# Performance work log

Measured on AMD Instinct MI355X. Metric: run time of the kernel, lower is better.

The kernel has to match this reference:

```python
import jax, jax.numpy as jnp
import numpy as np

B, SQ, SKV, D = 32, 1024, 8192, 64

def setup_inputs() -> dict:
    key = jax.random.key(0)
    kq, kk, kv = jax.random.split(key, 3)
    return {
        "q_local": jax.random.normal(kq, (B, SQ, D), dtype=jnp.float32),
        "k_local": jax.random.normal(kk, (B, SKV, D), dtype=jnp.float32),
        "v_local": jax.random.normal(kv, (B, SKV, D), dtype=jnp.float32),
    }

def reference(q_local, k_local, v_local):
    # Ring attention with online softmax over all ranks' K/V blocks is
    # mathematically identical to unscaled softmax(Q K^T) V over the full KV.
    scores = jnp.einsum("bqd,bkd->bqk", q_local, k_local)  # [B, SQ, SKV]
    weights = jax.nn.softmax(scores, axis=-1)              # stable (max-subtract)
    out = jnp.einsum("bqk,bkd->bqd", weights, v_local)
    return out.astype(q_local.dtype)
```

## Files before the change

kernel.cpp:

```cpp
#include <hip/hip_runtime.h>


#define NBATCH 32
#define SQL 1024
#define SKVL 8192
#define DH 64
#define BM 128
#define BN 64
#define KSTR 72
#define VSTR 72

typedef _Float16 half8 __attribute__((ext_vector_type(8)));
typedef __fp16 fp16x2 __attribute__((ext_vector_type(2)));
typedef float floatx16 __attribute__((ext_vector_type(16)));
typedef float floatx4 __attribute__((ext_vector_type(4)));
typedef unsigned int uint4v __attribute__((ext_vector_type(4)));
typedef unsigned int uint2v __attribute__((ext_vector_type(2)));

union F8U { uint4v u; half8 h; };

#if __has_builtin(__builtin_amdgcn_exp2f)
#define EXP2F(x) __builtin_amdgcn_exp2f(x)
#else
#define EXP2F(x) exp2f(x)
#endif

static __device__ __forceinline__ unsigned pk2(float a, float b) {
#if __has_builtin(__builtin_amdgcn_cvt_pkrtz)
  fp16x2 h = __builtin_amdgcn_cvt_pkrtz(a, b);
  return __builtin_bit_cast(unsigned, h);
#else
  union { _Float16 h[2]; unsigned u; } r;
  r.h[0] = (_Float16)a; r.h[1] = (_Float16)b; return r.u;
#endif
}

#if __has_builtin(__builtin_amdgcn_permlane32_swap)
#define HAVE_PL32 1
static __device__ __forceinline__ void pl32(unsigned& a, unsigned& b) {
  uint2v r = __builtin_amdgcn_permlane32_swap(a, b, false, false);
  a = r[0]; b = r[1];
}
#else
#define HAVE_PL32 0
#endif

template<int NSPLIT>
__global__ __launch_bounds__(256, 3)
void ring_attn(const float* __restrict__ q, const float* __restrict__ k,
               const float* __restrict__ v, float* __restrict__ out,
               float* __restrict__ pO, float* __restrict__ pM, float* __restrict__ pL)
{
  constexpr int NT = SKVL / NSPLIT / BN;
  __shared__ _Float16 Kl[2][BN * KSTR];
  __shared__ _Float16 Vt[2][DH * VSTR];

  const int tid  = threadIdx.x;
  const int lane = tid & 63;
  const int wv   = tid >> 6;
  const int l31  = lane & 31;
  const int hb   = lane >> 5;
  const int b8   = hb * 8;

  int split, batch, qb;
  if (NSPLIT == 4) {
    split = blockIdx.x & 3;
    batch = (blockIdx.x >> 2) & 31;
    qb    = blockIdx.x >> 7;
  } else {
    split = 0;
    batch = blockIdx.x & 31;
    qb    = blockIdx.x >> 5;
  }

  const float* kp = k + ((size_t)batch * SKVL + (size_t)split * (SKVL / NSPLIT)) * DH;
  const float* vp = v + ((size_t)batch * SKVL + (size_t)split * (SKVL / NSPLIT)) * DH;

  const float* qp = q + ((size_t)batch * SQL + qb * BM + wv * 32 + l31) * DH;
  half8 qf[4];
#pragma unroll
  for (int kt = 0; kt < 4; ++kt) {
    float4 a = *(const float4*)(qp + kt * 16 + b8);
    float4 c = *(const float4*)(qp + kt * 16 + b8 + 4);
    float xs[8] = {a.x, a.y, a.z, a.w, c.x, c.y, c.z, c.w};
#pragma unroll
    for (int j = 0; j < 8; ++j)
      qf[kt][j] = (_Float16)(xs[j] * 1.44269504088896340736f);
  }

  const int krt = tid >> 4;
  const int kc  = (tid & 15) * 4;
  const int vnr = 2 * (tid & 31);
  const int vcg = 8 * (tid >> 5);

  float4 gk[4], ga0, ga1, gb0, gb1;
#pragma unroll
  for (int it = 0; it < 4; ++it)
    gk[it] = *(const float4*)(kp + (size_t)(krt + it * 16) * DH + kc);
  ga0 = *(const float4*)(vp + (size_t)vnr * DH + vcg);
  ga1 = *(const float4*)(vp + (size_t)vnr * DH + vcg + 4);
  gb0 = *(const float4*)(vp + (size_t)(vnr + 1) * DH + vcg);
  gb1 = *(const float4*)(vp + (size_t)(vnr + 1) * DH + vcg + 4);

  floatx16 accO[2];
#pragma unroll
  for (int i = 0; i < 2; ++i)
#pragma unroll
    for (int r = 0; r < 16; ++r) accO[i][r] = 0.f;
  float m_run = -3.0e38f, l_run = 0.f;

  int buf = 0;
  for (int tile = 0; tile < NT; ++tile) {
    _Float16* Kb = Kl[buf];
    _Float16* Vb = Vt[buf];

#pragma unroll
    for (int it = 0; it < 4; ++it) {
      uint2 w2 = make_uint2(pk2(gk[it].x, gk[it].y), pk2(gk[it].z, gk[it].w));
      *(uint2*)&Kb[(krt + it * 16) * KSTR + kc] = w2;
    }
    {
      float av[8] = {ga0.x, ga0.y, ga0.z, ga0.w, ga1.x, ga1.y, ga1.z, ga1.w};
      float bv[8] = {gb0.x, gb0.y, gb0.z, gb0.w, gb1.x, gb1.y, gb1.z, gb1.w};
#pragma unroll
      for (int i = 0; i < 8; ++i)
        *(unsigned*)&Vb[(vcg + i) * VSTR + vnr] = pk2(av[i], bv[i]);
    }
    __syncthreads();

    if (tile + 1 < NT) {
      const float* kn = kp + (size_t)(tile + 1) * BN * DH;
      const float* vn = vp + (size_t)(tile + 1) * BN * DH;
#pragma unroll
      for (int it = 0; it < 4; ++it)
        gk[it] = *(const float4*)(kn + (size_t)(krt + it * 16) * DH + kc);
      ga0 = *(const float4*)(vn + (size_t)vnr * DH + vcg);
      ga1 = *(const float4*)(vn + (size_t)vnr * DH + vcg + 4);
      gb0 = *(const float4*)(vn + (size_t)(vnr + 1) * DH + vcg);
      gb1 = *(const float4*)(vn + (size_t)(vnr + 1) * DH + vcg + 4);
    }

    floatx16 st[2];
#pragma unroll
    for (int t = 0; t < 2; ++t)
#pragma unroll
      for (int r = 0; r < 16; ++r) st[t][r] = 0.f;
#pragma unroll
    for (int kt = 0; kt < 4; ++kt) {
#pragma unroll
      for (int t = 0; t < 2; ++t) {
        half8 kf = *(const half8*)&Kb[(t * 32 + l31) * KSTR + kt * 16 + b8];
        st[t] = __builtin_amdgcn_mfma_f32_32x32x16_f16(kf, qf[kt], st[t], 0, 0, 0);
      }
    }

    float mx = -3.0e38f;
#pragma unroll
    for (int t = 0; t < 2; ++t)
#pragma unroll
      for (int r = 0; r < 16; ++r) mx = fmaxf(mx, st[t][r]);
    mx = fmaxf(mx, __shfl_xor(mx, 32, 64));
    float m_new = fmaxf(m_run, mx);
    float alpha = EXP2F(m_run - m_new);
    m_run = m_new;
    float sum = 0.f;
#pragma unroll
    for (int t = 0; t < 2; ++t)
#pragma unroll
      for (int r = 0; r < 16; ++r) {
        float p = EXP2F(st[t][r] - m_new);
        st[t][r] = p;
        sum += p;
      }
    sum += __shfl_xor(sum, 32, 64);
    l_run = alpha * l_run + sum;

    if (__any(alpha != 1.0f)) {
#pragma unroll
      for (int r = 0; r < 16; ++r) {
        int row = (r & 3) + 8 * (r >> 2) + 4 * hb;
        float ar = __shfl(alpha, row, 64);
        accO[0][r] *= ar;
        accO[1][r] *= ar;
      }
    }

#pragma unroll
    for (int t = 0; t < 2; ++t) {
      unsigned P01 = pk2(st[t][0],  st[t][1]);
      unsigned P23 = pk2(st[t][2],  st[t][3]);
      unsigned P45 = pk2(st[t][4],  st[t][5]);
      unsigned P67 = pk2(st[t][6],  st[t][7]);
      unsigned P89 = pk2(st[t][8],  st[t][9]);
      unsigned PAB = pk2(st[t][10], st[t][11]);
      unsigned PCD = pk2(st[t][12], st[t][13]);
      unsigned PEF = pk2(st[t][14], st[t][15]);
      F8U fe, fo;
#if HAVE_PL32
      pl32(P01, P45); fe.u[0] = P01; fe.u[2] = P45;
      pl32(P23, P67); fe.u[1] = P23; fe.u[3] = P67;
      pl32(P89, PCD); fo.u[0] = P89; fo.u[2] = PCD;
      pl32(PAB, PEF); fo.u[1] = PAB; fo.u[3] = PEF;
#else
      unsigned x01 = __shfl_xor(P01, 32, 64), x23 = __shfl_xor(P23, 32, 64);
      unsigned x45 = __shfl_xor(P45, 32, 64), x67 = __shfl_xor(P67, 32, 64);
      unsigned x89 = __shfl_xor(P89, 32, 64), xAB = __shfl_xor(PAB, 32, 64);
      unsigned xCD = __shfl_xor(PCD, 32, 64), xEF = __shfl_xor(PEF, 32, 64);
      fe.u = uint4v{hb ? x45 : P01, hb ? x67 : P23, hb ? P45 : x01, hb ? P67 : x23};
      fo.u = uint4v{hb ? xCD : P89, hb ? xEF : PAB, hb ? PCD : x89, hb ? PEF : xAB};
#endif
#pragma unroll
      for (int ds = 0; ds < 2; ++ds) {
        half8 vf0 = *(const half8*)&Vb[(ds * 32 + l31) * VSTR + (2 * t) * 16 + b8];
        accO[ds] = __builtin_amdgcn_mfma_f32_32x32x16_f16(fe.h, vf0, accO[ds], 0, 0, 0);
        half8 vf1 = *(const half8*)&Vb[(ds * 32 + l31) * VSTR + (2 * t + 1) * 16 + b8];
        accO[ds] = __builtin_amdgcn_mfma_f32_32x32x16_f16(fo.h, vf1, accO[ds], 0, 0, 0);
      }
    }
    buf ^= 1;
  }

  const int rowbase = batch * SQL + qb * BM + wv * 32;
  if (NSPLIT == 1) {
    float linv = 1.0f / l_run;
    float* op = out + (size_t)rowbase * DH;
#pragma unroll
    for (int r = 0; r < 16; ++r) {
      int row = (r & 3) + 8 * (r >> 2) + 4 * hb;
      float lr = __shfl(linv, row, 64);
      op[(size_t)row * DH + l31]      = accO[0][r] * lr;
      op[(size_t)row * DH + 32 + l31] = accO[1][r] * lr;
    }
  } else {
    float* po = pO + ((size_t)split * NBATCH * SQL + rowbase) * DH;
#pragma unroll
    for (int r = 0; r < 16; ++r) {
      int row = (r & 3) + 8 * (r >> 2) + 4 * hb;
      po[(size_t)row * DH + l31]      = accO[0][r];
      po[(size_t)row * DH + 32 + l31] = accO[1][r];
    }
    if (hb == 0) {
      pM[(size_t)split * NBATCH * SQL + rowbase + l31] = m_run;
      pL[(size_t)split * NBATCH * SQL + rowbase + l31] = l_run;
    }
  }
}

__global__ __launch_bounds__(256)
void merge4(const float* __restrict__ pO, const float* __restrict__ pM,
            const float* __restrict__ pL, float* __restrict__ out)
{
  const int i4   = blockIdx.x * 256 + threadIdx.x;
  const int rowg = i4 >> 4;
  const size_t PLANE4 = (size_t)NBATCH * SQL * DH / 4;
  const int    RPL    = NBATCH * SQL;
  float m0 = pM[rowg], m1 = pM[RPL + rowg], m2 = pM[2 * RPL + rowg], m3 = pM[3 * RPL + rowg];
  float mx = fmaxf(fmaxf(m0, m1), fmaxf(m2, m3));
  float w0 = EXP2F(m0 - mx), w1 = EXP2F(m1 - mx), w2 = EXP2F(m2 - mx), w3 = EXP2F(m3 - mx);
  float l = w0 * pL[rowg] + w1 * pL[RPL + rowg] + w2 * pL[2 * RPL + rowg] + w3 * pL[3 * RPL + rowg];
  float li = 1.0f / l;
  const floatx4* p0 = (const floatx4*)pO;
  floatx4 o0 = p0[i4], o1 = p0[PLANE4 + i4], o2 = p0[2 * PLANE4 + i4], o3 = p0[3 * PLANE4 + i4];
  floatx4 o;
#pragma unroll
  for (int j = 0; j < 4; ++j)
    o[j] = (w0 * o0[j] + w1 * o1[j] + w2 * o2[j] + w3 * o3[j]) * li;
  ((floatx4*)out)[i4] = o;
}

extern "C" void kernel_launch(void* const* d_in, const int* in_sizes, int n_in,
                              void* d_out, int out_size, void* d_ws, size_t ws_size,
                              hipStream_t stream) {
  (void)in_sizes; (void)n_in; (void)out_size;
  const float* q = (const float*)d_in[0];
  const float* k = (const float*)d_in[1];
  const float* v = (const float*)d_in[2];
  float* out = (float*)d_out;

  const size_t PLANE = (size_t)NBATCH * SQL * DH;
  const size_t RPL   = (size_t)NBATCH * SQL;
  const size_t need  = (4 * PLANE + 8 * RPL) * sizeof(float);

  if (ws_size >= need) {
    float* pO = (float*)d_ws;
    float* pM = pO + 4 * PLANE;
    float* pL = pM + 4 * RPL;
    ring_attn<4><<<dim3(1024), dim3(256), 0, stream>>>(q, k, v, nullptr, pO, pM, pL);
    merge4<<<dim3((NBATCH * SQL * DH) / 1024), dim3(256), 0, stream>>>(pO, pM, pL, out);
  } else {
    ring_attn<1><<<dim3(256), dim3(256), 0, stream>>>(q, k, v, out, nullptr, nullptr, nullptr);
  }
}
```

Before: 251.9 us.

## Split softmax per 32-key subtile and stage prefetches as packed fp16 to raise occupancy

The online-softmax update now runs per 32-key half tile instead of per 64-key tile, so only one 16-float score accumulator is live at a time. Prefetched K/V values are converted to packed fp16 in registers early, and the V prefetch is staggered to the middle of the tile, lowering peak register pressure. Launch bounds rise from 3 to 4 blocks per SIMD-set to allow higher occupancy. In exchange there are twice as many max/rescale steps per tile, and the prefetch latency is hidden over a shorter window.

```diff
diff --git a/kernel.cpp b/kernel.cpp
--- a/kernel.cpp
+++ b/kernel.cpp
@@ -46,7 +46,7 @@
 #endif
 
 template<int NSPLIT>
-__global__ __launch_bounds__(256, 3)
+__global__ __launch_bounds__(256, 4)
 void ring_attn(const float* __restrict__ q, const float* __restrict__ k,
                const float* __restrict__ v, float* __restrict__ out,
                float* __restrict__ pO, float* __restrict__ pM, float* __restrict__ pL)
@@ -76,6 +76,28 @@
   const float* kp = k + ((size_t)batch * SKVL + (size_t)split * (SKVL / NSPLIT)) * DH;
   const float* vp = v + ((size_t)batch * SKVL + (size_t)split * (SKVL / NSPLIT)) * DH;
 
+  const int krt = tid >> 4;
+  const int kc  = (tid & 15) * 4;
+  const int vnr = 2 * (tid & 31);
+  const int vcg = 8 * (tid >> 5);
+
+  uint2 pkK[4]; unsigned pkV[8];
+  {
+#pragma unroll
+    for (int it = 0; it < 4; ++it) {
+      float4 g = *(const float4*)(kp + (size_t)(krt + it * 16) * DH + kc);
+      pkK[it] = make_uint2(pk2(g.x, g.y), pk2(g.z, g.w));
+    }
+    float4 a0 = *(const float4*)(vp + (size_t)vnr * DH + vcg);
+    float4 a1 = *(const float4*)(vp + (size_t)vnr * DH + vcg + 4);
+    float4 b0 = *(const float4*)(vp + (size_t)(vnr + 1) * DH + vcg);
+    float4 b1 = *(const float4*)(vp + (size_t)(vnr + 1) * DH + vcg + 4);
+    float av[8] = {a0.x, a0.y, a0.z, a0.w, a1.x, a1.y, a1.z, a1.w};
+    float bv[8] = {b0.x, b0.y, b0.z, b0.w, b1.x, b1.y, b1.z, b1.w};
+#pragma unroll
+    for (int i = 0; i < 8; ++i) pkV[i] = pk2(av[i], bv[i]);
+  }
+
   const float* qp = q + ((size_t)batch * SQL + qb * BM + wv * 32 + l31) * DH;
   half8 qf[4];
 #pragma unroll
@@ -88,20 +110,6 @@
       qf[kt][j] = (_Float16)(xs[j] * 1.44269504088896340736f);
   }
 
-  const int krt = tid >> 4;
-  const int kc  = (tid & 15) * 4;
-  const int vnr = 2 * (tid & 31);
-  const int vcg = 8 * (tid >> 5);
-
-  float4 gk[4], ga0, ga1, gb0, gb1;
-#pragma unroll
-  for (int it = 0; it < 4; ++it)
-    gk[it] = *(const float4*)(kp + (size_t)(krt + it * 16) * DH + kc);
-  ga0 = *(const float4*)(vp + (size_t)vnr * DH + vcg);
-  ga1 = *(const float4*)(vp + (size_t)vnr * DH + vcg + 4);
-  gb0 = *(const float4*)(vp + (size_t)(vnr + 1) * DH + vcg);
-  gb1 = *(const float4*)(vp + (size_t)(vnr + 1) * DH + vcg + 4);
-
   floatx16 accO[2];
 #pragma unroll
   for (int i = 0; i < 2; ++i)
@@ -109,92 +117,87 @@
     for (int r = 0; r < 16; ++r) accO[i][r] = 0.f;
   float m_run = -3.0e38f, l_run = 0.f;
 
+  float4 gk[4], gv[4];
   int buf = 0;
   for (int tile = 0; tile < NT; ++tile) {
     _Float16* Kb = Kl[buf];
     _Float16* Vb = Vt[buf];
 
 #pragma unroll
-    for (int it = 0; it < 4; ++it) {
-      uint2 w2 = make_uint2(pk2(gk[it].x, gk[it].y), pk2(gk[it].z, gk[it].w));
-      *(uint2*)&Kb[(krt + it * 16) * KSTR + kc] = w2;
-    }
-    {
-      float av[8] = {ga0.x, ga0.y, ga0.z, ga0.w, ga1.x, ga1.y, ga1.z, ga1.w};
-      float bv[8] = {gb0.x, gb0.y, gb0.z, gb0.w, gb1.x, gb1.y, gb1.z, gb1.w};
-#pragma unroll
-      for (int i = 0; i < 8; ++i)
-        *(unsigned*)&Vb[(vcg + i) * VSTR + vnr] = pk2(av[i], bv[i]);
-    }
+    for (int it = 0; it < 4; ++it)
+      *(uint2*)&Kb[(krt + it * 16) * KSTR + kc] = pkK[it];
+#pragma unroll
+    for (int i = 0; i < 8; ++i)
+      *(unsigned*)&Vb[(vcg + i) * VSTR + vnr] = pkV[i];
     __syncthreads();
 
-    if (tile + 1 < NT) {
+    const bool more = (tile + 1 < NT);
+    if (more) {
       const float* kn = kp + (size_t)(tile + 1) * BN * DH;
-      const float* vn = vp + (size_t)(tile + 1) * BN * DH;
 #pragma unroll
       for (int it = 0; it < 4; ++it)
         gk[it] = *(const float4*)(kn + (size_t)(krt + it * 16) * DH + kc);
-      ga0 = *(const float4*)(vn + (size_t)vnr * DH + vcg);
-      ga1 = *(const float4*)(vn + (size_t)vnr * DH + vcg + 4);
-      gb0 = *(const float4*)(vn + (size_t)(vnr + 1) * DH + vcg);
-      gb1 = *(const float4*)(vn + (size_t)(vnr + 1) * DH + vcg + 4);
-    }
-
-    floatx16 st[2];
-#pragma unroll
-    for (int t = 0; t < 2; ++t)
-#pragma unroll
-      for (int r = 0; r < 16; ++r) st[t][r] = 0.f;
-#pragma unroll
-    for (int kt = 0; kt < 4; ++kt) {
-#pragma unroll
-      for (int t = 0; t < 2; ++t) {
+    }
+
+#pragma unroll
+    for (int t = 0; t < 2; ++t) {
+      floatx16 stv;
+#pragma unroll
+      for (int r = 0; r < 16; ++r) stv[r] = 0.f;
+#pragma unroll
+      for (int kt = 0; kt < 4; ++kt) {
         half8 kf = *(const half8*)&Kb[(t * 32 + l31) * KSTR + kt * 16 + b8];
-        st[t] = __builtin_amdgcn_mfma_f32_32x32x16_f16(kf, qf[kt], st[t], 0, 0, 0);
-      }
-    }
-
-    float mx = -3.0e38f;
-#pragma unroll
-    for (int t = 0; t < 2; ++t)
-#pragma unroll
-      for (int r = 0; r < 16; ++r) mx = fmaxf(mx, st[t][r]);
-    mx = fmaxf(mx, __shfl_xor(mx, 32, 64));
-    float m_new = fmaxf(m_run, mx);
-    float alpha = EXP2F(m_run - m_new);
-    m_run = m_new;
-    float sum = 0.f;
-#pragma unroll
-    for (int t = 0; t < 2; ++t)
+        stv = __builtin_amdgcn_mfma_f32_32x32x16_f16(kf, qf[kt], stv, 0, 0, 0);
+      }
+
+      float mx = stv[0];
+#pragma unroll
+      for (int r = 1; r < 16; ++r) mx = fmaxf(mx, stv[r]);
+      mx = fmaxf(mx, __shfl_xor(mx, 32, 64));
+      float m_new = fmaxf(m_run, mx);
+      float alpha = EXP2F(m_run - m_new);
+      m_run = m_new;
+      float sum = 0.f;
 #pragma unroll
       for (int r = 0; r < 16; ++r) {
-        float p = EXP2F(st[t][r] - m_new);
-        st[t][r] = p;
+        float p = EXP2F(stv[r] - m_new);
+        stv[r] = p;
         sum += p;
       }
-    sum += __shfl_xor(sum, 32, 64);
-    l_run = alpha * l_run + sum;
-
-    if (__any(alpha != 1.0f)) {
-#pragma unroll
-      for (int r = 0; r < 16; ++r) {
-        int row = (r & 3) + 8 * (r >> 2) + 4 * hb;
-        float ar = __shfl(alpha, row, 64);
-        accO[0][r] *= ar;
-        accO[1][r] *= ar;
-      }
-    }
-
-#pragma unroll
-    for (int t = 0; t < 2; ++t) {
-      unsigned P01 = pk2(st[t][0],  st[t][1]);
-      unsigned P23 = pk2(st[t][2],  st[t][3]);
-      unsigned P45 = pk2(st[t][4],  st[t][5]);
-      unsigned P67 = pk2(st[t][6],  st[t][7]);
-      unsigned P89 = pk2(st[t][8],  st[t][9]);
-      unsigned PAB = pk2(st[t][10], st[t][11]);
-      unsigned PCD = pk2(st[t][12], st[t][13]);
-      unsigned PEF = pk2(st[t][14], st[t][15]);
+      sum += __shfl_xor(sum, 32, 64);
+      l_run = alpha * l_run + sum;
+      if (__any(alpha != 1.0f)) {
+#pragma unroll
+        for (int r = 0; r < 16; ++r) {
+          int row = (r & 3) + 8 * (r >> 2) + 4 * hb;
+          float ar = __shfl(alpha, row, 64);
+          accO[0][r] *= ar;
+          accO[1][r] *= ar;
+        }
+      }
+
+      if (more) {
+        if (t == 0) {
+#pragma unroll
+          for (int it = 0; it < 4; ++it)
+            pkK[it] = make_uint2(pk2(gk[it].x, gk[it].y), pk2(gk[it].z, gk[it].w));
+          const float* vn = vp + (size_t)(tile + 1) * BN * DH;
+          gv[0] = *(const float4*)(vn + (size_t)vnr * DH + vcg);
+          gv[1] = *(const float4*)(vn + (size_t)vnr * DH + vcg + 4);
+          gv[2] = *(const float4*)(vn + (size_t)(vnr + 1) * DH + vcg);
+          gv[3] = *(const float4*)(vn + (size_t)(vnr + 1) * DH + vcg + 4);
+        } else {
+          float av[8] = {gv[0].x, gv[0].y, gv[0].z, gv[0].w, gv[1].x, gv[1].y, gv[1].z, gv[1].w};
+          float bv[8] = {gv[2].x, gv[2].y, gv[2].z, gv[2].w, gv[3].x, gv[3].y, gv[3].z, gv[3].w};
+#pragma unroll
+          for (int i = 0; i < 8; ++i) pkV[i] = pk2(av[i], bv[i]);
+        }
+      }
+
+      unsigned P01 = pk2(stv[0],  stv[1]),  P23 = pk2(stv[2],  stv[3]);
+      unsigned P45 = pk2(stv[4],  stv[5]),  P67 = pk2(stv[6],  stv[7]);
+      unsigned P89 = pk2(stv[8],  stv[9]),  PAB = pk2(stv[10], stv[11]);
+      unsigned PCD = pk2(stv[12], stv[13]), PEF = pk2(stv[14], stv[15]);
       F8U fe, fo;
 #if HAVE_PL32
       pl32(P01, P45); fe.u[0] = P01; fe.u[2] = P45;
```

Result: slower. 273.5 us (+8.6%).
